# Optimization experiments

Measured on AMD Instinct MI355X. Metric: run time of the kernel, lower is better.

Reference implementation:

```python
import jax, jax.numpy as jnp
import numpy as np

MIN_DURATION = 0.0
MAX_DURATION = 75.0
MAX_LEN = 80  # hard-coded output length from regulate_length's slice/pad to 80
LN_EPS = 1e-6


def _conv1d_same(x, w, b):
    # x: [B, T, Cin], w: [K, Cin, Cout] -> [B, T, Cout]
    y = jax.lax.conv_general_dilated(
        x, w, window_strides=(1,), padding='SAME',
        dimension_numbers=('NWC', 'WIO', 'NWC'))
    return y + b


def _layernorm(x, gamma, beta):
    mu = jnp.mean(x, axis=-1, keepdims=True)
    var = jnp.mean(jnp.square(x - mu), axis=-1, keepdims=True)
    return (x - mu) * jax.lax.rsqrt(var + LN_EPS) * gamma + beta


def setup_inputs() -> dict:
    key = jax.random.key(0)
    ks = jax.random.split(key, 5)
    B, T, D, F, K = 2048, 128, 256, 256, 3
    scale = 0.05
    return {
        'encoder_output': jax.random.normal(ks[0], (B, T, D), jnp.float32),
        'conv1_w': jax.random.normal(ks[1], (K, D, F), jnp.float32) * scale,
        'conv1_b': jnp.zeros((F,), jnp.float32),
        'conv2_w': jax.random.normal(ks[2], (K, F, F), jnp.float32) * scale,
        'conv2_b': jnp.zeros((F,), jnp.float32),
        'ln_gamma': jnp.ones((F,), jnp.float32),
        'ln_beta': jnp.zeros((F,), jnp.float32),
        'dense_w': jax.random.normal(ks[3], (F, 1), jnp.float32) * scale,
        'dense_b': jnp.full((1,), 2.0, jnp.float32),  # bias so rounded durations are nontrivial
    }


def reference(encoder_output, conv1_w, conv1_b, conv2_w, conv2_b,
              ln_gamma, ln_beta, dense_w, dense_b):
    # --- variance predictor (dropout = identity at inference) ---
    x = jax.nn.relu(_conv1d_same(encoder_output, conv1_w, conv1_b))
    x = _layernorm(x, ln_gamma, ln_beta)
    x = jax.nn.relu(_conv1d_same(x, conv2_w, conv2_b))
    x = _layernorm(x, ln_gamma, ln_beta)
    predicted_durations = x @ dense_w + dense_b  # [B, T, 1]

    # --- regulate_length, fully vectorized over batch ---
    dur = jnp.round(jnp.clip(predicted_durations, MIN_DURATION, MAX_DURATION))
    dur = dur[..., 0].astype(jnp.int32)                 # [B, T]
    cum = jnp.cumsum(dur, axis=1)                       # [B, T]
    pos = jnp.arange(MAX_LEN, dtype=jnp.int32)          # [80]
    # source index for each output frame: searchsorted(cum, pos, side='right')
    idx = jnp.sum(pos[None, :, None] >= cum[:, None, :], axis=-1)  # [B, 80]
    valid = pos[None, :] < cum[:, -1:]                  # [B, 80]
    T = encoder_output.shape[1]
    gathered = jnp.take_along_axis(
        encoder_output, jnp.clip(idx, 0, T - 1)[..., None], axis=1)  # [B, 80, D]
    regulated = jnp.where(valid[..., None], gathered, 0.0)
    return regulated
```

## Files before the change

### kernel.cpp

```cpp
#include <hip/hip_runtime.h>
#include <hip/hip_bf16.h>
#include <math.h>

#define TT 128
#define CC 256
#define MAXLEN 80
#define KSTEPS 24
#define SLOTS 130
#define NCH16 32

typedef __attribute__((ext_vector_type(8))) _Float16 half8v;
typedef __attribute__((ext_vector_type(2))) _Float16 half2v;
typedef __attribute__((ext_vector_type(4))) float f32x4;

#define MSCALE 4096.0f
#define MINV   (1.0f/4096.0f)

__device__ __forceinline__ int chunkidx(int slot, int c16) {
    return slot * NCH16 + (c16 ^ (slot & 7));
}

__device__ __forceinline__ void split2(float x0, float x1, half2v& h, half2v& m) {
    h = __builtin_bit_cast(half2v, __builtin_amdgcn_cvt_pkrtz(x0, x1));
    m.x = (_Float16)fmaf((float)h.x, -MSCALE, x0 * MSCALE);
    m.y = (_Float16)fmaf((float)h.y, -MSCALE, x1 * MSCALE);
}

__global__ void va_prep(const float* __restrict__ w1, const float* __restrict__ w2,
                        half8v* __restrict__ wsB)
{
    const int idx = blockIdx.x * 256 + threadIdx.x;
    const int lane = idx & 63;
    int q = idx >> 6;
    const int nfg = q & 15;   q >>= 4;
    const int plane = q & 1;  q >>= 1;
    const int kk2 = q & 7;    q >>= 3;
    const int tap = q % 3;
    const int cv  = q / 3;
    const float* w = cv ? w2 : w1;
    const int co  = nfg * 16 + (lane & 15);
    const int ci0 = kk2 * 32 + (lane >> 4) * 8;
    half8v out;
    #pragma unroll
    for (int j = 0; j < 8; ++j) {
        const float x = w[tap * (CC * CC) + (ci0 + j) * CC + co];
        const _Float16 h = (_Float16)x;
        if (plane == 0) out[j] = h;
        else            out[j] = (_Float16)((x - (float)h) * MSCALE);
    }
    wsB[idx] = out;
}

__global__ __launch_bounds__(512, 2)
void va_mfma(const float* __restrict__ enc,
             const float* __restrict__ b1g, const float* __restrict__ b2g,
             const float* __restrict__ gg,  const float* __restrict__ bbg,
             const float* __restrict__ dwg, const float* __restrict__ dbg,
             const half8v* __restrict__ wsB,
             float* __restrict__ outg)
{
    __shared__ half8v P[2][SLOTS * NCH16];
    __shared__ float sumS[4][TT];
    __shared__ float sumQ[4][TT];
    __shared__ float muS[TT];
    __shared__ float rsS[TT];
    __shared__ int   durS[TT];
    __shared__ int   cumS[TT];
    __shared__ int   wtotS[2];

    const int b    = blockIdx.x;
    const int tid  = threadIdx.x;
    const int wid  = tid >> 6;
    const int lane = tid & 63;
    const int l15  = lane & 15;
    const int lg   = lane >> 4;
    const int MGr  = (wid >> 2) * 64;
    const int NG   = wid & 3;
    const int NGc  = NG * 64;

    const f32x4* encB4 = reinterpret_cast<const f32x4*>(enc) + (size_t)b * (TT * 64);

    for (int m2 = tid; m2 < SLOTS * NCH16; m2 += 512) {
        const int slot = m2 >> 5;
        const int c16  = m2 & 31;
        half8v h8, m8;
        if (slot >= 1 && slot <= TT) {
            const f32x4* src = encB4 + (slot - 1) * 64 + c16 * 2;
            const f32x4 v0 = src[0], v1 = src[1];
            half2v hp, mp;
            split2(v0.x, v0.y, hp, mp); h8[0]=hp.x; h8[1]=hp.y; m8[0]=mp.x; m8[1]=mp.y;
            split2(v0.z, v0.w, hp, mp); h8[2]=hp.x; h8[3]=hp.y; m8[2]=mp.x; m8[3]=mp.y;
            split2(v1.x, v1.y, hp, mp); h8[4]=hp.x; h8[5]=hp.y; m8[4]=mp.x; m8[5]=mp.y;
            split2(v1.z, v1.w, hp, mp); h8[6]=hp.x; h8[7]=hp.y; m8[6]=mp.x; m8[7]=mp.y;
        } else {
            #pragma unroll
            for (int j = 0; j < 8; ++j) { h8[j] = (_Float16)0.f; m8[j] = (_Float16)0.f; }
        }
        const int ci = chunkidx(slot, c16);
        P[0][ci] = h8;
        P[1][ci] = m8;
    }
    __syncthreads();

    f32x4 accH[4][4];
    f32x4 accM[4][4];

    float gv[4], bvv[4];
    #pragma unroll
    for (int nf = 0; nf < 4; ++nf) {
        gv[nf]  = gg[NGc + nf * 16 + l15];
        bvv[nf] = bbg[NGc + nf * 16 + l15];
    }

    auto convpass = [&](int cv, const float* __restrict__ biasp, bool first) {
        #pragma unroll
        for (int nf = 0; nf < 4; ++nf) {
            const float bz = biasp[NGc + nf * 16 + l15];
            const f32x4 b4 = {bz, bz, bz, bz};
            const f32x4 z4 = {0.f, 0.f, 0.f, 0.f};
            #pragma unroll
            for (int mf = 0; mf < 4; ++mf) { accH[mf][nf] = b4; accM[mf][nf] = z4; }
        }

        half8v B0[8], B1[8];
        auto loadB = [&](half8v (&Bp)[8], int ks) {
            const int tap = ks >> 3, kk2 = ks & 7;
            const int fb = ((cv * 3 + tap) * 8 + kk2) * 2;
            #pragma unroll
            for (int p = 0; p < 2; ++p)
                #pragma unroll
                for (int nf = 0; nf < 4; ++nf)
                    Bp[p * 4 + nf] = wsB[(size_t)((fb + p) * 16 + (NG * 4 + nf)) * 64 + lane];
        };
        auto doK = [&](const half8v (&Bp)[8], int ks) {
            const int tap = ks >> 3, kk2 = ks & 7;
            #pragma unroll
            for (int mf = 0; mf < 4; ++mf) {
                const int slot = MGr + mf * 16 + l15 + tap;
                const int c16  = kk2 * 4 + lg;
                const int ci = chunkidx(slot, c16);
                const half8v Ah = P[0][ci];
                const half8v Am = P[1][ci];
                #pragma unroll
                for (int nf = 0; nf < 4; ++nf) {
                    accH[mf][nf] = __builtin_amdgcn_mfma_f32_16x16x32_f16(Ah, Bp[nf],     accH[mf][nf], 0, 0, 0);
                    accM[mf][nf] = __builtin_amdgcn_mfma_f32_16x16x32_f16(Ah, Bp[4 + nf], accM[mf][nf], 0, 0, 0);
                    accM[mf][nf] = __builtin_amdgcn_mfma_f32_16x16x32_f16(Am, Bp[nf],     accM[mf][nf], 0, 0, 0);
                }
            }
        };

        loadB(B0, 0);
        #pragma unroll 1
        for (int ks = 0; ks < KSTEPS; ks += 2) {
            loadB(B1, ks + 1);
            doK(B0, ks);
            if (ks + 2 < KSTEPS) loadB(B0, ks + 2);
            doK(B1, ks + 1);
        }

        #pragma unroll
        for (int mf = 0; mf < 4; ++mf)
            #pragma unroll
            for (int nf = 0; nf < 4; ++nf) {
                f32x4 v;
                #pragma unroll
                for (int e = 0; e < 4; ++e)
                    v[e] = fmaxf(fmaf(accM[mf][nf][e], MINV, accH[mf][nf][e]), 0.f);
                accH[mf][nf] = v;
            }

        #pragma unroll
        for (int mf = 0; mf < 4; ++mf)
            #pragma unroll
            for (int r = 0; r < 4; ++r) {
                float s = (accH[mf][0][r] + accH[mf][1][r]) + (accH[mf][2][r] + accH[mf][3][r]);
                float q = accH[mf][0][r] * accH[mf][0][r];
                q = fmaf(accH[mf][1][r], accH[mf][1][r], q);
                q = fmaf(accH[mf][2][r], accH[mf][2][r], q);
                q = fmaf(accH[mf][3][r], accH[mf][3][r], q);
                #pragma unroll
                for (int o = 1; o < 16; o <<= 1) {
                    s += __shfl_xor(s, o, 64);
                    q += __shfl_xor(q, o, 64);
                }
                if (l15 == 0) {
                    const int row = MGr + mf * 16 + lg * 4 + r;
                    sumS[NG][row] = s;
                    sumQ[NG][row] = q;
                }
            }
        __syncthreads();
        if (tid < TT) {
            const float S = (sumS[0][tid] + sumS[1][tid]) + (sumS[2][tid] + sumS[3][tid]);
            const float Q = (sumQ[0][tid] + sumQ[1][tid]) + (sumQ[2][tid] + sumQ[3][tid]);
            const float mu = S * (1.f / 256.f);
            const float var = fmaf(-mu, mu, Q * (1.f / 256.f));
            muS[tid] = mu;
            rsS[tid] = 1.0f / sqrtf(var + 1e-6f);
        }
        __syncthreads();
        _Float16* Ph = (_Float16*)&P[0][0];
        _Float16* Pm = (_Float16*)&P[1][0];
        #pragma unroll
        for (int mf = 0; mf < 4; ++mf)
            #pragma unroll
            for (int r = 0; r < 4; ++r) {
                const int row = MGr + mf * 16 + lg * 4 + r;
                const float mu = muS[row];
                const float rs = rsS[row];
                #pragma unroll
                for (int nf = 0; nf < 4; ++nf) {
                    const float v = (accH[mf][nf][r] - mu) * rs * gv[nf] + bvv[nf];
                    if (first) {
                        const int col = NGc + nf * 16 + l15;
                        const int slot = row + 1;
                        const int off = chunkidx(slot, col >> 3) * 8 + (col & 7);
                        const _Float16 h = (_Float16)v;
                        Ph[off] = h;
                        Pm[off] = (_Float16)fmaf((float)h, -MSCALE, v * MSCALE);
                    } else {
                        accH[mf][nf][r] = v;
                    }
                }
            }
    };

    convpass(0, b1g, true);
    __syncthreads();
    convpass(1, b2g, false);

    {
        float dv[4];
        #pragma unroll
        for (int nf = 0; nf < 4; ++nf) dv[nf] = dwg[NGc + nf * 16 + l15];
        #pragma unroll
        for (int mf = 0; mf < 4; ++mf)
            #pragma unroll
            for (int r = 0; r < 4; ++r) {
                float p = (accH[mf][0][r] * dv[0] + accH[mf][1][r] * dv[1])
                        + (accH[mf][2][r] * dv[2] + accH[mf][3][r] * dv[3]);
                #pragma unroll
                for (int o = 1; o < 16; o <<= 1) p += __shfl_xor(p, o, 64);
                if (l15 == 0) sumS[NG][MGr + mf * 16 + lg * 4 + r] = p;
            }
        __syncthreads();
        if (tid < TT) {
            const float pd = (sumS[0][tid] + sumS[1][tid]) + (sumS[2][tid] + sumS[3][tid]) + dbg[0];
            const float dcl = fminf(fmaxf(pd, 0.0f), 75.0f);
            durS[tid] = (int)rintf(dcl);
        }
        __syncthreads();
    }

    int sv = 0;
    if (tid < TT) {
        sv = durS[tid];
        #pragma unroll
        for (int o = 1; o < 64; o <<= 1) {
            const int u = __shfl_up(sv, o, 64);
            if (lane >= o) sv += u;
        }
        if (lane == 63) wtotS[tid >> 6] = sv;
    }
    __syncthreads();
    if (tid < TT) {
        if (tid >= 64) sv += wtotS[0];
        cumS[tid] = sv;
    }
    __syncthreads();

    const int total = cumS[TT - 1];
    f32x4* outB4 = reinterpret_cast<f32x4*>(outg) + (size_t)b * (MAXLEN * 64);
    for (int pp = 0; pp < 10; ++pp) {
        const int p = wid * 10 + pp;
        int lo = 0, hi = TT;
        while (lo < hi) {
            const int mid = (lo + hi) >> 1;
            if (cumS[mid] <= p) lo = mid + 1; else hi = mid;
        }
        f32x4 v = {0.f, 0.f, 0.f, 0.f};
        if (p < total) {
            const int src = (lo < TT) ? lo : (TT - 1);
            v = encB4[src * 64 + lane];
        }
        outB4[p * 64 + lane] = v;
    }
}

extern "C" void kernel_launch(void* const* d_in, const int* in_sizes, int n_in,
                              void* d_out, int out_size, void* d_ws, size_t ws_size,
                              hipStream_t stream) {
    const float* enc = (const float*)d_in[0];
    const float* w1  = (const float*)d_in[1];
    const float* b1  = (const float*)d_in[2];
    const float* w2  = (const float*)d_in[3];
    const float* b2  = (const float*)d_in[4];
    const float* gam = (const float*)d_in[5];
    const float* bet = (const float*)d_in[6];
    const float* dw  = (const float*)d_in[7];
    const float* db  = (const float*)d_in[8];
    float* out = (float*)d_out;
    half8v* wsB = (half8v*)d_ws;

    const int B = in_sizes[0] / (TT * CC);
    hipLaunchKernelGGL(va_prep, dim3(384), dim3(256), 0, stream, w1, w2, wsB);
    hipLaunchKernelGGL(va_mfma, dim3(B), dim3(512), 0, stream,
                       enc, b1, b2, gam, bet, dw, db, wsB, out);
}
```

Measured before the change: 654.7 us.

## Split each batch into two time halves with halo recompute and separate gather kernel

Each batch's 128 time steps are processed by two 256-thread blocks of 64 rows each, recomputing conv1 halo rows (padded to 80 rows) so conv2 needs no cross-block data. Durations are written to workspace and a separate kernel does the cumsum and gather. This halves LDS per block so more blocks can co-reside and overlap their barrier phases, at the cost of extra conv1 MFMA work and an additional launch plus global round-trip for durations.

New measurement: 633.2 us. 1.03x faster.

```diff
diff --git a/kernel.cpp b/kernel.cpp
--- a/kernel.cpp
+++ b/kernel.cpp
@@ -6,7 +6,7 @@
 #define CC 256
 #define MAXLEN 80
 #define KSTEPS 24
-#define SLOTS 130
+#define SLOTS 68
 #define NCH16 32
 
 typedef __attribute__((ext_vector_type(8))) _Float16 half8v;
@@ -51,41 +51,39 @@
     wsB[idx] = out;
 }
 
-__global__ __launch_bounds__(512, 2)
-void va_mfma(const float* __restrict__ enc,
+__global__ __launch_bounds__(256, 2)
+void va_conv(const float* __restrict__ enc,
              const float* __restrict__ b1g, const float* __restrict__ b2g,
              const float* __restrict__ gg,  const float* __restrict__ bbg,
              const float* __restrict__ dwg, const float* __restrict__ dbg,
              const half8v* __restrict__ wsB,
-             float* __restrict__ outg)
+             int* __restrict__ durG)
 {
     __shared__ half8v P[2][SLOTS * NCH16];
-    __shared__ float sumS[4][TT];
-    __shared__ float sumQ[4][TT];
-    __shared__ float muS[TT];
-    __shared__ float rsS[TT];
-    __shared__ int   durS[TT];
-    __shared__ int   cumS[TT];
-    __shared__ int   wtotS[2];
-
-    const int b    = blockIdx.x;
+    __shared__ float sumS[4][80];
+    __shared__ float sumQ[4][80];
+    __shared__ float muS[80];
+    __shared__ float rsS[80];
+
+    const int bb   = blockIdx.x;
+    const int b    = bb >> 1;
+    const int base = (bb & 1) << 6;
     const int tid  = threadIdx.x;
     const int wid  = tid >> 6;
     const int lane = tid & 63;
     const int l15  = lane & 15;
     const int lg   = lane >> 4;
-    const int MGr  = (wid >> 2) * 64;
-    const int NG   = wid & 3;
-    const int NGc  = NG * 64;
+    const int NGc  = wid * 64;
 
     const f32x4* encB4 = reinterpret_cast<const f32x4*>(enc) + (size_t)b * (TT * 64);
 
-    for (int m2 = tid; m2 < SLOTS * NCH16; m2 += 512) {
+    for (int m2 = tid; m2 < SLOTS * NCH16; m2 += 256) {
         const int slot = m2 >> 5;
         const int c16  = m2 & 31;
+        const int ra   = base + slot - 2;
         half8v h8, m8;
-        if (slot >= 1 && slot <= TT) {
-            const f32x4* src = encB4 + (slot - 1) * 64 + c16 * 2;
+        if (ra >= 0 && ra < TT) {
+            const f32x4* src = encB4 + ra * 64 + c16 * 2;
             const f32x4 v0 = src[0], v1 = src[1];
             half2v hp, mp;
             split2(v0.x, v0.y, hp, mp); h8[0]=hp.x; h8[1]=hp.y; m8[0]=mp.x; m8[1]=mp.y;
@@ -102,9 +100,6 @@
     }
     __syncthreads();
 
-    f32x4 accH[4][4];
-    f32x4 accM[4][4];
-
     float gv[4], bvv[4];
     #pragma unroll
     for (int nf = 0; nf < 4; ++nf) {
@@ -112,33 +107,134 @@
         bvv[nf] = bbg[NGc + nf * 16 + l15];
     }
 
-    auto convpass = [&](int cv, const float* __restrict__ biasp, bool first) {
+    f32x4 accH[5][4];
+    f32x4 accM[5][4];
+
+    {
+        const int F1[5] = {-1, 15, 31, 47, 49};
         #pragma unroll
         for (int nf = 0; nf < 4; ++nf) {
-            const float bz = biasp[NGc + nf * 16 + l15];
+            const float bz = b1g[NGc + nf * 16 + l15];
             const f32x4 b4 = {bz, bz, bz, bz};
             const f32x4 z4 = {0.f, 0.f, 0.f, 0.f};
             #pragma unroll
+            for (int mf = 0; mf < 5; ++mf) { accH[mf][nf] = b4; accM[mf][nf] = z4; }
+        }
+        #pragma unroll 1
+        for (int ks = 0; ks < KSTEPS; ++ks) {
+            const int tap = ks >> 3, kk2 = ks & 7;
+            half8v B[8];
+            {
+                const int fb = (tap * 8 + kk2) * 2;
+                #pragma unroll
+                for (int p = 0; p < 2; ++p)
+                    #pragma unroll
+                    for (int nf = 0; nf < 4; ++nf)
+                        B[p * 4 + nf] = wsB[(size_t)((fb + p) * 16 + (wid * 4 + nf)) * 64 + lane];
+            }
+            #pragma unroll
+            for (int mf = 0; mf < 5; ++mf) {
+                const int slot = F1[mf] + l15 + tap + 1;
+                const int ci = chunkidx(slot, kk2 * 4 + lg);
+                const half8v Ah = P[0][ci];
+                const half8v Am = P[1][ci];
+                #pragma unroll
+                for (int nf = 0; nf < 4; ++nf) {
+                    accH[mf][nf] = __builtin_amdgcn_mfma_f32_16x16x32_f16(Ah, B[nf],     accH[mf][nf], 0, 0, 0);
+                    accM[mf][nf] = __builtin_amdgcn_mfma_f32_16x16x32_f16(Ah, B[4 + nf], accM[mf][nf], 0, 0, 0);
+                    accM[mf][nf] = __builtin_amdgcn_mfma_f32_16x16x32_f16(Am, B[nf],     accM[mf][nf], 0, 0, 0);
+                }
+            }
+        }
+        #pragma unroll
+        for (int mf = 0; mf < 5; ++mf)
+            #pragma unroll
+            for (int nf = 0; nf < 4; ++nf) {
+                f32x4 v;
+                #pragma unroll
+                for (int e = 0; e < 4; ++e)
+                    v[e] = fmaxf(fmaf(accM[mf][nf][e], MINV, accH[mf][nf][e]), 0.f);
+                accH[mf][nf] = v;
+            }
+        #pragma unroll
+        for (int mf = 0; mf < 5; ++mf)
+            #pragma unroll
+            for (int r = 0; r < 4; ++r) {
+                float s = (accH[mf][0][r] + accH[mf][1][r]) + (accH[mf][2][r] + accH[mf][3][r]);
+                float q = accH[mf][0][r] * accH[mf][0][r];
+                q = fmaf(accH[mf][1][r], accH[mf][1][r], q);
+                q = fmaf(accH[mf][2][r], accH[mf][2][r], q);
+                q = fmaf(accH[mf][3][r], accH[mf][3][r], q);
+                #pragma unroll
+                for (int o = 1; o < 16; o <<= 1) {
+                    s += __shfl_xor(s, o, 64);
+                    q += __shfl_xor(q, o, 64);
+                }
+                if (l15 == 0) {
+                    const int idx = F1[mf] + lg * 4 + r + 1;
+                    sumS[wid][idx] = s;
+                    sumQ[wid][idx] = q;
+                }
+            }
+        __syncthreads();
+        if (tid < 66) {
+            const float S = (sumS[0][tid] + sumS[1][tid]) + (sumS[2][tid] + sumS[3][tid]);
+            const float Q = (sumQ[0][tid] + sumQ[1][tid]) + (sumQ[2][tid] + sumQ[3][tid]);
+            const float mu = S * (1.f / 256.f);
+            const float var = fmaf(-mu, mu, Q * (1.f / 256.f));
+            muS[tid] = mu;
+            rsS[tid] = 1.0f / sqrtf(var + 1e-6f);
+        }
+        __syncthreads();
+        _Float16* Ph = (_Float16*)&P[0][0];
+        _Float16* Pm = (_Float16*)&P[1][0];
+        #pragma unroll
+        for (int mf = 0; mf < 5; ++mf)
+            #pragma unroll
+            for (int r = 0; r < 4; ++r) {
+                const int row = F1[mf] + lg * 4 + r;
+                const float mu = muS[row + 1];
+                const float rs = rsS[row + 1];
+                const bool valid = (base + row >= 0) && (base + row < TT);
+                #pragma unroll
+                for (int nf = 0; nf < 4; ++nf) {
+                    float v = (accH[mf][nf][r] - mu) * rs * gv[nf] + bvv[nf];
+                    if (!valid) v = 0.f;
+                    const int col = NGc + nf * 16 + l15;
+                    const int off = chunkidx(row + 2, col >> 3) * 8 + (col & 7);
+                    const _Float16 h = (_Float16)v;
+                    Ph[off] = h;
+                    Pm[off] = (_Float16)fmaf((float)h, -MSCALE, v * MSCALE);
+                }
+            }
+    }
+    __syncthreads();
+
+    {
+        #pragma unroll
+        for (int nf = 0; nf < 4; ++nf) {
+            const float bz = b2g[NGc + nf * 16 + l15];
+            const f32x4 b4 = {bz, bz, bz, bz};
+            const f32x4 z4 = {0.f, 0.f, 0.f, 0.f};
+            #pragma unroll
             for (int mf = 0; mf < 4; ++mf) { accH[mf][nf] = b4; accM[mf][nf] = z4; }
         }
-
         half8v B0[8], B1[8];
         auto loadB = [&](half8v (&Bp)[8], int ks) {
             const int tap = ks >> 3, kk2 = ks & 7;
-            const int fb = ((cv * 3 + tap) * 8 + kk2) * 2;
+            const int fb = ((3 + tap) * 8 + kk2) * 2;
             #pragma unroll
             for (int p = 0; p < 2; ++p)
                 #pragma unroll
                 for (int nf = 0; nf < 4; ++nf)
-                    Bp[p * 4 + nf] = wsB[(size_t)((fb + p) * 16 + (NG * 4 + nf)) * 64 + lane];
+                    Bp[p * 4 + nf] = wsB[(size_t)((fb + p) * 16 + (wid * 4 + nf)) * 64 + lane];
         };
         auto doK = [&](const half8v (&Bp)[8], int ks) {
             const int tap = ks >> 3, kk2 = ks & 7;
             #pragma unroll
             for (int mf = 0; mf < 4; ++mf) {
-                const int slot = MGr + mf * 16 + l15 + tap;
-                const int c16  = kk2 * 4 + lg;
-                const int ci = chunkidx(slot, c16);
+                const int slot = mf * 16 + l15 + tap + 1;
+                const int ci = chunkidx(slot, kk2 * 4 + lg);
                 const half8v Ah = P[0][ci];
                 const half8v Am = P[1][ci];
                 #pragma unroll
@@ -149,7 +245,6 @@
                 }
             }
         };
-
         loadB(B0, 0);
         #pragma unroll 1
         for (int ks = 0; ks < KSTEPS; ks += 2) {
@@ -158,7 +253,6 @@
             if (ks + 2 < KSTEPS) loadB(B0, ks + 2);
             doK(B1, ks + 1);
         }
-
         #pragma unroll
         for (int mf = 0; mf < 4; ++mf)
             #pragma unroll
@@ -169,7 +263,6 @@
                     v[e] = fmaxf(fmaf(accM[mf][nf][e], MINV, accH[mf][nf][e]), 0.f);
                 accH[mf][nf] = v;
             }
-
         #pragma unroll
         for (int mf = 0; mf < 4; ++mf)
             #pragma unroll
@@ -185,13 +278,13 @@
                     q += __shfl_xor(q, o, 64);
                 }
                 if (l15 == 0) {
-                    const int row = MGr + mf * 16 + lg * 4 + r;
-                    sumS[NG][row] = s;
-                    sumQ[NG][row] = q;
-                }
-            }
-        __syncthreads();
-        if (tid < TT) {
+                    const int idx = mf * 16 + lg * 4 + r;
+                    sumS[wid][idx] = s;
+                    sumQ[wid][idx] = q;
+                }
+            }
+        __syncthreads();
+        if (tid < 64) {
             const float S = (sumS[0][tid] + sumS[1][tid]) + (sumS[2][tid] + sumS[3][tid]);
             const float Q = (sumQ[0][tid] + sumQ[1][tid]) + (sumQ[2][tid] + sumQ[3][tid]);
             const float mu = S * (1.f / 256.f);
@@ -200,62 +293,49 @@
             rsS[tid] = 1.0f / sqrtf(var + 1e-6f);
         }
         __syncthreads();
-        _Float16* Ph = (_Float16*)&P[0][0];
-        _Float16* Pm = (_Float16*)&P[1][0];
+        float dv[4];
+        #pragma unroll
+        for (int nf = 0; nf < 4; ++nf) dv[nf] = dwg[NGc + nf * 16 + l15];
         #pragma unroll
         for (int mf = 0; mf < 4; ++mf)
             #pragma unroll
             for (int r = 0; r < 4; ++r) {
-                const int row = MGr + mf * 16 + lg * 4 + r;
+                const int row = mf * 16 + lg * 4 + r;
                 const float mu = muS[row];
                 const float rs = rsS[row];
+                float p = 0.f;
                 #pragma unroll
                 for (int nf = 0; nf < 4; ++nf) {
                     const float v = (accH[mf][nf][r] - mu) * rs * gv[nf] + bvv[nf];
-                    if (first) {
-                        const int col = NGc + nf * 16 + l15;
-                        const int slot = row + 1;
-                        const int off = chunkidx(slot, col >> 3) * 8 + (col & 7);
-                        const _Float16 h = (_Float16)v;
-                        Ph[off] = h;
-                        Pm[off] = (_Float16)fmaf((float)h, -MSCALE, v * MSCALE);
-                    } else {
-                        accH[mf][nf][r] = v;
-                    }
-                }
-            }
-    };
-
-    convpass(0, b1g, true);
-    __syncthreads();
-    convpass(1, b2g, false);
-
-    {
-        float dv[4];
-        #pragma unroll
-        for (int nf = 0; nf < 4; ++nf) dv[nf] = dwg[NGc + nf * 16 + l15];
-        #pragma unroll
-        for (int mf = 0; mf < 4; ++mf)
-            #pragma unroll
-            for (int r = 0; r < 4; ++r) {
-                float p = (accH[mf][0][r] * dv[0] + accH[mf][1][r] * dv[1])
-                        + (accH[mf][2][r] * dv[2] + accH[mf][3][r] * dv[3]);
+                    p = fmaf(v, dv[nf], p);
+                }
                 #pragma unroll
                 for (int o = 1; o < 16; o <<= 1) p += __shfl_xor(p, o, 64);
-                if (l15 == 0) sumS[NG][MGr + mf * 16 + lg * 4 + r] = p;
-            }
-        __syncthreads();
-        if (tid < TT) {
+                if (l15 == 0) sumS[wid][row] = p;
+            }
+        __syncthreads();
+        if (tid < 64) {
             const float pd = (sumS[0][tid] + sumS[1][tid]) + (sumS[2][tid] + sumS[3][tid]) + dbg[0];
             const float dcl = fminf(fmaxf(pd, 0.0f), 75.0f);
-            durS[tid] = (int)rintf(dcl);
-        }
-        __syncthreads();
-    }
+            durG[b * TT + base + tid] = (int)rintf(dcl);
+        }
+    }
+}
+
+__global__ __launch_bounds__(256)
+void va_gather(const float* __restrict__ enc, const int* __restrict__ durG,
+               float* __restrict__ outg)
+{
+    __shared__ int cumS[TT];
+    __shared__ int wtotS[2];
+    const int b    = blockIdx.x;
+    const int tid  = threadIdx.x;
+    const int wid  = tid >> 6;
+    const int lane = tid & 63;
 
     int sv = 0;
     if (tid < TT) {
-        sv = durS[tid];
+        sv = durG[b * TT + tid];
         #pragma unroll
         for (int o = 1; o < 64; o <<= 1) {
             const int u = __shfl_up(sv, o, 64);
@@ -271,9 +351,10 @@
     __syncthreads();
 
     const int total = cumS[TT - 1];
+    const f32x4* encB4 = reinterpret_cast<const f32x4*>(enc) + (size_t)b * (TT * 64);
     f32x4* outB4 = reinterpret_cast<f32x4*>(outg) + (size_t)b * (MAXLEN * 64);
-    for (int pp = 0; pp < 10; ++pp) {
-        const int p = wid * 10 + pp;
+    for (int pp = 0; pp < 20; ++pp) {
+        const int p = wid * 20 + pp;
         int lo = 0, hi = TT;
         while (lo < hi) {
             const int mid = (lo + hi) >> 1;
@@ -302,9 +383,11 @@
     const float* db  = (const float*)d_in[8];
     float* out = (float*)d_out;
     half8v* wsB = (half8v*)d_ws;
+    int* durG = (int*)((char*)d_ws + 98304u * 16u);
 
     const int B = in_sizes[0] / (TT * CC);
     hipLaunchKernelGGL(va_prep, dim3(384), dim3(256), 0, stream, w1, w2, wsB);
-    hipLaunchKernelGGL(va_mfma, dim3(B), dim3(512), 0, stream,
-                       enc, b1, b2, gam, bet, dw, db, wsB, out);
-}
+    hipLaunchKernelGGL(va_conv, dim3(B * 2), dim3(256), 0, stream,
+                       enc, b1, b2, gam, bet, dw, db, wsB, durG);
+    hipLaunchKernelGGL(va_gather, dim3(B), dim3(256), 0, stream, enc, durG, out);
+}
```
